# Kernel tuning notes

Hardware: AMD Instinct MI355X
Metric: run time of the kernel (lower is better)

Reference implementation:

```python
import jax, jax.numpy as jnp
import numpy as np

GRID_SIZE = 5
SPLINE_ORDER = 3
ALPHA = 0.2


def _make_grid(in_features, dtype=jnp.float32):
    # uniform grid on [-1, 1] extended by spline_order on each side
    h = 2.0 / GRID_SIZE
    pts = jnp.arange(-SPLINE_ORDER, GRID_SIZE + SPLINE_ORDER + 1, dtype=dtype) * h - 1.0
    return jnp.broadcast_to(pts, (in_features, pts.shape[0]))  # [in, G+2k+1]


def _b_splines(x, grid):
    # x: [N, in] -> bases: [N, in, GRID_SIZE + SPLINE_ORDER]
    x = x[..., None]  # [N, in, 1]
    bases = ((x >= grid[:, :-1]) & (x < grid[:, 1:])).astype(x.dtype)
    for k in range(1, SPLINE_ORDER + 1):
        left = (x - grid[:, : -(k + 1)]) / (grid[:, k:-1] - grid[:, : -(k + 1)])
        right = (grid[:, k + 1 :] - x) / (grid[:, k + 1 :] - grid[:, 1:-k])
        bases = left * bases[..., :-1] + right * bases[..., 1:]
    return bases


def _kan(x, base_weight, spline_weight):
    # efficient-KAN layer: silu base linear + B-spline linear
    N, Fin = x.shape
    Fout = base_weight.shape[0]
    grid = _make_grid(Fin, x.dtype)
    bases = _b_splines(x, grid)  # [N, in, C]
    base_out = jax.nn.silu(x) @ base_weight.T
    spline_out = bases.reshape(N, -1) @ spline_weight.reshape(Fout, -1).T
    return base_out + spline_out


def setup_inputs() -> dict:
    key = jax.random.key(0)
    k1, k2, k3, k4, k5, k6 = jax.random.split(key, 6)
    N, E, Fin, Fout = 50000, 800000, 128, 128
    C = GRID_SIZE + SPLINE_ORDER
    h = jax.random.normal(k1, (N, Fin), dtype=jnp.float32)
    edge_index = jax.random.randint(k2, (2, E), 0, N, dtype=jnp.int64)
    W = jax.random.normal(k3, (Fin, Fout), dtype=jnp.float32) * (1.414 / np.sqrt(Fin))
    a = jax.random.normal(k4, (2 * Fout, 1), dtype=jnp.float32) * 0.1
    base_weight = jax.random.normal(k5, (Fout, Fin), dtype=jnp.float32) / np.sqrt(Fin)
    spline_weight = jax.random.normal(k6, (Fout, Fin, C), dtype=jnp.float32) * 0.1
    return {"h": h, "edge_index": edge_index, "W": W, "a": a,
            "base_weight": base_weight, "spline_weight": spline_weight}


def reference(h, edge_index, W, a, base_weight, spline_weight):
    N = h.shape[0]
    Fout = W.shape[1]
    HW = h @ W                                # [N, Fout]
    HW_KAN = _kan(h, base_weight, spline_weight)  # [N, Fout]
    row, col = edge_index[0], edge_index[1]
    # cat([HW_i, HW_j]) @ a == HW_i @ a[:Fout] + HW_j @ a[Fout:]; precompute per node
    s_src = HW @ a[:Fout, 0]                  # [N]
    s_dst = HW @ a[Fout:, 0]                  # [N]
    e = jax.nn.leaky_relu(s_src[row] + s_dst[col], ALPHA)  # [E]
    # segment softmax grouped by row
    m = jax.ops.segment_max(e, row, num_segments=N)
    e_exp = jnp.exp(e - m[row])
    denom = jax.ops.segment_sum(e_exp, row, num_segments=N)
    att = e_exp / denom[row]                  # [E] (dropout inactive in eval)
    out = jax.ops.segment_sum(att[:, None] * HW_KAN[col], row, num_segments=N)
    return out
```

## Files before the change

### kernel.cpp

```cpp
#include <hip/hip_runtime.h>
#include <hip/hip_bf16.h>
#include <math.h>

#define NCHUNK 9
#define BM 128
#define NTHR 512
#define PREPB ((NCHUNK * 128 * 128) / 256)

typedef __attribute__((ext_vector_type(4))) float f32x4;
typedef __attribute__((ext_vector_type(8))) short bf16x8;
typedef unsigned int u32;
typedef unsigned long long u64;

__device__ __forceinline__ unsigned short f2bf(float f) {
    u32 u = __builtin_bit_cast(u32, f);
    u32 r = (u + 0x7FFFu + ((u >> 16) & 1u)) >> 16;
    return (unsigned short)r;
}

__device__ __forceinline__ float siluf(float x) {
    return x / (1.0f + __expf(-x));
}

__global__ void k_prep(const float* __restrict__ bw, const float* __restrict__ sw,
                       const float* __restrict__ W, const float* __restrict__ a,
                       unsigned short* __restrict__ Bsw, float* __restrict__ wa,
                       const int* __restrict__ erow, int* __restrict__ counts, int E) {
    int bid = blockIdx.x;
    if (bid < PREPB) {
        int i = bid * 256 + threadIdx.x;
        int j = i & 7;
        int s = (i >> 3) & 15;
        int o = (i >> 7) & 127;
        int c = i >> 14;
        int k = c * 128 + (((s ^ (o & 7)) << 3) | j);
        float v = (k < 128) ? bw[o * 128 + k] : sw[o * 1024 + (k - 128)];
        Bsw[i] = f2bf(v);
        return;
    }
    if (bid == PREPB) {
        int fi = threadIdx.x;
        if (fi < 128) {
            float s1 = 0.f, s2 = 0.f;
            for (int o = 0; o < 128; ++o) {
                float w = W[fi * 128 + o];
                s1 = fmaf(w, a[o], s1);
                s2 = fmaf(w, a[128 + o], s2);
            }
            wa[fi] = s1;
            wa[128 + fi] = s2;
        }
        return;
    }
    int e = (bid - PREPB - 1) * 256 + threadIdx.x;
    if (e < E) atomicAdd(&counts[erow[e]], 1);
}

__global__ __launch_bounds__(NTHR) void k_nodes(const float* __restrict__ h,
                                                const unsigned short* __restrict__ Bsw,
                                                const float* __restrict__ wa,
                                                unsigned short* __restrict__ kanb,
                                                float* __restrict__ s_src,
                                                float* __restrict__ s_dst, int N, int nbn,
                                                const int* __restrict__ erow,
                                                const int* __restrict__ ecol,
                                                const int* __restrict__ offsets,
                                                int* __restrict__ cursor,
                                                int* __restrict__ colss, int E) {
    __shared__ unsigned short A_lds[BM * 128];
    __shared__ unsigned short B_lds[128 * 128];
    const int tid = threadIdx.x;

    if (blockIdx.x >= nbn) {
        int e = (blockIdx.x - nbn) * NTHR + tid;
        if (e < E) {
            int r = erow[e];
            int pos = offsets[r] + atomicAdd(&cursor[r], 1);
            colss[pos] = ecol[e];
        }
        return;
    }

    const int wid = tid >> 6, lane = tid & 63;
    const int gm0 = blockIdx.x * BM;

    const int gm = tid >> 2, gq = tid & 3;
    const float* ghr = h + (size_t)min(gm0 + gm, N - 1) * 128;

    const int wm0 = (wid >> 1) * 32;
    const int wn0 = (wid & 1) * 64;
    f32x4 acc[2][4];
#pragma unroll
    for (int im = 0; im < 2; ++im)
#pragma unroll
        for (int in = 0; in < 4; ++in) acc[im][in] = {0.f, 0.f, 0.f, 0.f};

    f32x4 pf = {0.f, 0.f, 0.f, 0.f};
    for (int chunk = 0; chunk < NCHUNK; ++chunk) {
        {
            const char* gsrc = (const char*)Bsw + (size_t)chunk * 32768 + wid * 4096 + lane * 16;
            char* ldst = (char*)B_lds + wid * 4096;
#pragma unroll
            for (int i = 0; i < 4; ++i) {
                __builtin_amdgcn_global_load_lds(
                    (const __attribute__((address_space(1))) u32*)(gsrc + i * 1024),
                    (__attribute__((address_space(3))) u32*)(ldst + i * 1024), 16, 0, 0);
            }
        }
        f32x4 pfn = pf;
        if (chunk <= 7) pfn = *(const f32x4*)(ghr + chunk * 16 + gq * 4);

        if (chunk == 0) {
            f32x4 xv[8];
#pragma unroll
            for (int v = 0; v < 8; ++v) xv[v] = *(const f32x4*)(ghr + gq * 32 + v * 4);
#pragma unroll
            for (int sl = 0; sl < 4; ++sl) {
                int s = gq * 4 + sl;
                unsigned short pk[8];
#pragma unroll
                for (int j = 0; j < 4; ++j) {
                    pk[j] = f2bf(siluf(xv[2 * sl][j]));
                    pk[4 + j] = f2bf(siluf(xv[2 * sl + 1][j]));
                }
                *(bf16x8*)((char*)A_lds + gm * 256 + (((s ^ (gm & 7)) & 15) << 4)) =
                    *(bf16x8*)pk;
            }
        } else {
#pragma unroll
            for (int j = 0; j < 4; ++j) {
                float x = pf[j];
                float t = (x + 2.2f) * 2.5f;
                float fl = floorf(t);
                int i0 = (int)fl;
                float u = t - fl;
                float um = 1.0f - u;
                float u2 = u * u, u3 = u2 * u;
                const float c6 = 1.0f / 6.0f;
                float w0 = um * um * um * c6;
                float w1 = (3.f * u3 - 6.f * u2 + 4.f) * c6;
                float w2 = (-3.f * u3 + 3.f * u2 + 3.f * u + 1.f) * c6;
                float w3 = u3 * c6;
                u64 Wp = (u64)f2bf(w0) | ((u64)f2bf(w1) << 16) |
                         ((u64)f2bf(w2) << 32) | ((u64)f2bf(w3) << 48);
                int sh = (i0 - 3) * 16;
                u64 lo = 0, hi = 0;
                if (sh >= 0) {
                    if (sh < 64) {
                        lo = Wp << sh;
                        hi = sh ? (Wp >> (64 - sh)) : 0;
                    } else if (sh < 128) {
                        hi = Wp << (sh - 64);
                    }
                } else {
                    int r = -sh;
                    if (r < 64) lo = Wp >> r;
                }
                int s = gq * 4 + j;
                ulonglong2 pv; pv.x = lo; pv.y = hi;
                *(ulonglong2*)((char*)A_lds + gm * 256 + (((s ^ (gm & 7)) & 15) << 4)) = pv;
            }
        }
        __syncthreads();

#pragma unroll
        for (int kk = 0; kk < 4; ++kk) {
            bf16x8 af[2], bfr[4];
#pragma unroll
            for (int im = 0; im < 2; ++im) {
                int mrow = wm0 + im * 16 + (lane & 15);
                int slot = (kk * 4 + (lane >> 4)) ^ (mrow & 7);
                af[im] = *(const bf16x8*)((const char*)A_lds + mrow * 256 + slot * 16);
            }
#pragma unroll
            for (int in = 0; in < 4; ++in) {
                int orow = wn0 + in * 16 + (lane & 15);
                int slot = (kk * 4 + (lane >> 4)) ^ (orow & 7);
                bfr[in] = *(const bf16x8*)((const char*)B_lds + orow * 256 + slot * 16);
            }
#pragma unroll
            for (int im = 0; im < 2; ++im)
#pragma unroll
                for (int in = 0; in < 4; ++in)
                    acc[im][in] = __builtin_amdgcn_mfma_f32_16x16x32_bf16(
                        af[im], bfr[in], acc[im][in], 0, 0, 0);
        }
        __syncthreads();
        pf = pfn;
    }

    float wa0 = wa[lane], wa1 = wa[64 + lane];
    float wa2 = wa[128 + lane], wa3 = wa[192 + lane];
    float sx0[16], sx1[16];
    const int r0 = gm0 + wid * 16;
#pragma unroll
    for (int rr = 0; rr < 16; ++rr) {
        const float* hr = h + (size_t)min(r0 + rr, N - 1) * 128;
        sx0[rr] = hr[lane];
        sx1[rr] = hr[64 + lane];
    }

#pragma unroll
    for (int im = 0; im < 2; ++im) {
        int rbase = wm0 + im * 16 + ((lane >> 4) << 2);
#pragma unroll
        for (int in = 0; in < 4; ++in) {
            int col = wn0 + in * 16 + (lane & 15);
#pragma unroll
            for (int r = 0; r < 4; ++r) {
                int row = rbase + r;
                int byte = row * 256 + ((col * 2) ^ ((row & 7) << 4));
                *(unsigned short*)((char*)A_lds + byte) = f2bf(acc[im][in][r]);
            }
        }
    }
    __syncthreads();
    for (int i = tid; i < BM * 16; i += NTHR) {
        int row = i >> 4, s = i & 15;
        int byte = row * 256 + ((s << 4) ^ ((row & 7) << 4));
        bf16x8 v = *(bf16x8*)((char*)A_lds + byte);
        int grow = gm0 + row;
        if (grow < N) *(bf16x8*)((char*)kanb + (size_t)grow * 256 + s * 16) = v;
    }

#pragma unroll
    for (int rr = 0; rr < 16; ++rr) {
        float s1 = fmaf(sx0[rr], wa0, sx1[rr] * wa1);
        float s2 = fmaf(sx0[rr], wa2, sx1[rr] * wa3);
#pragma unroll
        for (int off = 32; off; off >>= 1) {
            s1 += __shfl_xor(s1, off, 64);
            s2 += __shfl_xor(s2, off, 64);
        }
        int grow = r0 + rr;
        if (lane == 0 && grow < N) {
            s_src[grow] = s1;
            s_dst[grow] = s2;
        }
    }
}

__global__ void k_scan1(const int* __restrict__ counts, int* __restrict__ bsum, int N) {
    int tid = threadIdx.x;
    int idx = blockIdx.x * 256 + tid;
    int v = (idx < N) ? counts[idx] : 0;
#pragma unroll
    for (int off = 32; off; off >>= 1) v += __shfl_xor(v, off, 64);
    __shared__ int ws[4];
    if ((tid & 63) == 0) ws[tid >> 6] = v;
    __syncthreads();
    if (tid == 0) bsum[blockIdx.x] = ws[0] + ws[1] + ws[2] + ws[3];
}

__global__ __launch_bounds__(1024) void k_scan2(const int* __restrict__ bsum,
                                                int* __restrict__ ebase,
                                                int* __restrict__ offsN, int nb) {
    __shared__ int ws[16];
    __shared__ int tot;
    int tid = threadIdx.x;
    int lane = tid & 63, w = tid >> 6;
    int v = (tid < nb) ? bsum[tid] : 0;
    int inc = v;
#pragma unroll
    for (int off = 1; off < 64; off <<= 1) {
        int t = __shfl_up(inc, off, 64);
        if (lane >= off) inc += t;
    }
    if (lane == 63) ws[w] = inc;
    __syncthreads();
    if (w == 0 && lane < 16) {
        int x = ws[lane];
#pragma unroll
        for (int off = 1; off < 16; off <<= 1) {
            int t = __shfl_up(x, off, 64);
            if (lane >= off) x += t;
        }
        ws[lane] = x;
        if (lane == 15) tot = x;
    }
    __syncthreads();
    int wb = w ? ws[w - 1] : 0;
    if (tid < nb) ebase[tid] = wb + inc - v;
    if (tid == 0) offsN[0] = tot;
}

__global__ void k_scan3(const int* __restrict__ counts, const int* __restrict__ ebase,
                        int* __restrict__ offsets, int N) {
    int tid = threadIdx.x;
    int idx = blockIdx.x * 256 + tid;
    int v = (idx < N) ? counts[idx] : 0;
    int lane = tid & 63, w = tid >> 6;
    int inc = v;
#pragma unroll
    for (int off = 1; off < 64; off <<= 1) {
        int t = __shfl_up(inc, off, 64);
        if (lane >= off) inc += t;
    }
    __shared__ int ws[4];
    if (lane == 63) ws[w] = inc;
    __syncthreads();
    int wb = 0;
    for (int i = 0; i < w; ++i) wb += ws[i];
    if (idx < N) offsets[idx] = ebase[blockIdx.x] + wb + inc - v;
}

__global__ __launch_bounds__(256) void k_aggr(const int* __restrict__ offsets,
                                              int* __restrict__ cols,
                                              const float* __restrict__ s_src,
                                              const float* __restrict__ s_dst,
                                              const unsigned short* __restrict__ kanb,
                                              float* __restrict__ out, int N) {
    int wid = (blockIdx.x * 256 + threadIdx.x) >> 6;
    int lane = threadIdx.x & 63;
    if (wid >= N) return;
    int start = offsets[wid], end = offsets[wid + 1];
    int deg = end - start;
    float acc0 = 0.f, acc1 = 0.f;
    if (deg > 0) {
        float ssrc = s_src[wid];
        if (deg <= 64) {
            int key = 0x7fffffff;
            if (lane < deg) key = cols[start + lane];
#pragma unroll
            for (int k = 2; k <= 64; k <<= 1) {
#pragma unroll
                for (int j = k >> 1; j > 0; j >>= 1) {
                    int other = __shfl_xor(key, j, 64);
                    bool asc = ((lane & k) == 0);
                    bool lowr = ((lane & j) == 0);
                    int mn = min(key, other), mx = max(key, other);
                    key = (asc == lowr) ? mn : mx;
                }
            }
            float e = -3.402823466e38f;
            if (lane < deg) {
                e = ssrc + s_dst[key];
                e = (e >= 0.f) ? e : 0.2f * e;
            }
            float m = e;
#pragma unroll
            for (int off = 32; off; off >>= 1) m = fmaxf(m, __shfl_xor(m, off, 64));
            float ex = (lane < deg) ? __expf(e - m) : 0.f;
            float s = ex;
#pragma unroll
            for (int off = 32; off; off >>= 1) s += __shfl_xor(s, off, 64);
            float att = ex / s;
            for (int q0 = 0; q0 < deg; q0 += 4) {
                float w[4];
                u32 p[4];
#pragma unroll
                for (int t = 0; t < 4; ++t) {
                    int q = q0 + t;
                    int c = __shfl(key, q < deg ? q : 0, 64);
                    float wt = __shfl(att, q < 64 ? q : 0, 64);
                    w[t] = (q < deg) ? wt : 0.f;
                    p[t] = ((const u32*)(kanb + (size_t)c * 128))[lane];
                }
#pragma unroll
                for (int t = 0; t < 4; ++t) {
                    float lo = __builtin_bit_cast(float, p[t] << 16);
                    float hi = __builtin_bit_cast(float, p[t] & 0xffff0000u);
                    acc0 = fmaf(w[t], lo, acc0);
                    acc1 = fmaf(w[t], hi, acc1);
                }
            }
        } else {
            if (lane == 0) {
                for (int i = start + 1; i < end; ++i) {
                    int v = cols[i];
                    int j = i - 1;
                    while (j >= start && cols[j] > v) { cols[j + 1] = cols[j]; --j; }
                    cols[j + 1] = v;
                }
            }
            __threadfence();
            float m = -3.402823466e38f;
            for (int j = start + lane; j < end; j += 64) {
                float e = ssrc + s_dst[cols[j]];
                e = (e >= 0.f) ? e : 0.2f * e;
                m = fmaxf(m, e);
            }
#pragma unroll
            for (int off = 32; off; off >>= 1) m = fmaxf(m, __shfl_xor(m, off, 64));
            float s = 0.f;
            for (int j = start + lane; j < end; j += 64) {
                float e = ssrc + s_dst[cols[j]];
                e = (e >= 0.f) ? e : 0.2f * e;
                s += __expf(e - m);
            }
#pragma unroll
            for (int off = 32; off; off >>= 1) s += __shfl_xor(s, off, 64);
            float inv = 1.0f / s;
            for (int t = start; t < end; t += 64) {
                int j = t + lane;
                float att = 0.f;
                int myc = 0;
                if (j < end) {
                    myc = cols[j];
                    float e = ssrc + s_dst[myc];
                    e = (e >= 0.f) ? e : 0.2f * e;
                    att = __expf(e - m) * inv;
                }
                int cnt = min(64, end - t);
                for (int q = 0; q < cnt; ++q) {
                    float w = __shfl(att, q, 64);
                    int c = __shfl(myc, q, 64);
                    u32 p = ((const u32*)(kanb + (size_t)c * 128))[lane];
                    float lo = __builtin_bit_cast(float, p << 16);
                    float hi = __builtin_bit_cast(float, p & 0xffff0000u);
                    acc0 = fmaf(w, lo, acc0);
                    acc1 = fmaf(w, hi, acc1);
                }
            }
        }
    }
    float2 o2 = make_float2(acc0, acc1);
    *(float2*)(out + (size_t)wid * 128 + lane * 2) = o2;
}

extern "C" void kernel_launch(void* const* d_in, const int* in_sizes, int n_in,
                              void* d_out, int out_size, void* d_ws, size_t ws_size,
                              hipStream_t stream) {
    const float* h  = (const float*)d_in[0];
    const int*   ei = (const int*)d_in[1];
    const float* W  = (const float*)d_in[2];
    const float* a  = (const float*)d_in[3];
    const float* bw = (const float*)d_in[4];
    const float* sw = (const float*)d_in[5];
    float* out = (float*)d_out;
    const int N = in_sizes[0] / 128;
    const int E = in_sizes[1] / 2;
    const int nb = (N + 255) / 256;
    const int nbn = (N + BM - 1) / BM;
    const int nbs = (E + NTHR - 1) / NTHR;
    const int nbh = (E + 255) / 256;

    char* ws = (char*)d_ws;
    auto alloc = [&](size_t bytes) {
        char* p = ws;
        ws += (bytes + 255) & ~(size_t)255;
        return p;
    };
    unsigned short* Bsw = (unsigned short*)alloc((size_t)NCHUNK * 128 * 128 * 2);
    float* wa    = (float*)alloc(256 * 4);
    float* ssrc  = (float*)alloc((size_t)N * 4);
    float* sdst  = (float*)alloc((size_t)N * 4);
    unsigned short* kanb = (unsigned short*)alloc((size_t)N * 128 * 2);
    int* counts  = (int*)alloc((size_t)N * 4);
    int* cursor  = (int*)alloc((size_t)N * 4);
    int* offsets = (int*)alloc(((size_t)N + 1) * 4);
    int* colss   = (int*)alloc((size_t)E * 4);
    int* bsum    = (int*)alloc((size_t)nb * 4);
    int* ebase   = (int*)alloc((size_t)nb * 4);

    hipMemsetAsync(counts, 0, (size_t)N * 4, stream);
    hipMemsetAsync(cursor, 0, (size_t)N * 4, stream);

    k_prep<<<PREPB + 1 + nbh, 256, 0, stream>>>(bw, sw, W, a, Bsw, wa, ei, counts, E);
    k_scan1<<<nb, 256, 0, stream>>>(counts, bsum, N);
    k_scan2<<<1, 1024, 0, stream>>>(bsum, ebase, offsets + N, nb);
    k_scan3<<<nb, 256, 0, stream>>>(counts, ebase, offsets, N);
    k_nodes<<<nbn + nbs, NTHR, 0, stream>>>(h, Bsw, wa, kanb, ssrc, sdst, N, nbn,
                                            ei, ei + E, offsets, cursor, colss, E);
    k_aggr<<<(N + 3) / 4, 256, 0, stream>>>(offsets, colss, ssrc, sdst, kanb, out, N);
}
```

Measured before the change: 148.3 us.

## Software-pipeline neighbor gathers, change LDS swizzle, merge memsets

The aggregation loop now gathers neighbor features in batches of 8 and prefetches the next batch while the current one is accumulated, so more global loads are in flight to hide gather latency. The LDS XOR swizzle used when staging the KAN output tile is changed to a pattern keyed on row groups, aimed at fewer bank conflicts on the bf16 stores and reads. The two memsets of counts and cursor are merged into one call, relying on the two buffers being contiguous in the workspace. The prefetch raises register pressure and issues extra padded loads when degree is below 8.

```diff
diff --git a/kernel.cpp b/kernel.cpp
--- a/kernel.cpp
+++ b/kernel.cpp
@@ -209,7 +209,7 @@
 #pragma unroll
             for (int r = 0; r < 4; ++r) {
                 int row = rbase + r;
-                int byte = row * 256 + ((col * 2) ^ ((row & 7) << 4));
+                int byte = row * 256 + ((col * 2) ^ (((row >> 2) & 3) << 5));
                 *(unsigned short*)((char*)A_lds + byte) = f2bf(acc[im][in][r]);
             }
         }
@@ -217,7 +217,7 @@
     __syncthreads();
     for (int i = tid; i < BM * 16; i += NTHR) {
         int row = i >> 4, s = i & 15;
-        int byte = row * 256 + ((s << 4) ^ ((row & 7) << 4));
+        int byte = row * 256 + ((s << 4) ^ (((row >> 2) & 3) << 5));
         bf16x8 v = *(bf16x8*)((char*)A_lds + byte);
         int grow = gm0 + row;
         if (grow < N) *(bf16x8*)((char*)kanb + (size_t)grow * 256 + s * 16) = v;
@@ -345,23 +345,36 @@
 #pragma unroll
             for (int off = 32; off; off >>= 1) s += __shfl_xor(s, off, 64);
             float att = ex / s;
-            for (int q0 = 0; q0 < deg; q0 += 4) {
-                float w[4];
-                u32 p[4];
-#pragma unroll
-                for (int t = 0; t < 4; ++t) {
-                    int q = q0 + t;
-                    int c = __shfl(key, q < deg ? q : 0, 64);
-                    float wt = __shfl(att, q < 64 ? q : 0, 64);
-                    w[t] = (q < deg) ? wt : 0.f;
-                    p[t] = ((const u32*)(kanb + (size_t)c * 128))[lane];
-                }
-#pragma unroll
-                for (int t = 0; t < 4; ++t) {
-                    float lo = __builtin_bit_cast(float, p[t] << 16);
-                    float hi = __builtin_bit_cast(float, p[t] & 0xffff0000u);
-                    acc0 = fmaf(w[t], lo, acc0);
-                    acc1 = fmaf(w[t], hi, acc1);
+            u32 pbuf[8];
+            float wbuf[8];
+#pragma unroll
+            for (int t = 0; t < 8; ++t) {
+                int qc = (t < deg) ? t : 0;
+                int c = __shfl(key, qc, 64);
+                wbuf[t] = (t < deg) ? __shfl(att, qc, 64) : 0.f;
+                pbuf[t] = ((const u32*)(kanb + (size_t)c * 128))[lane];
+            }
+            for (int q0 = 0; q0 < deg; q0 += 8) {
+                u32 pc[8];
+                float wc[8];
+#pragma unroll
+                for (int t = 0; t < 8; ++t) { pc[t] = pbuf[t]; wc[t] = wbuf[t]; }
+                if (q0 + 8 < deg) {
+#pragma unroll
+                    for (int t = 0; t < 8; ++t) {
+                        int q = q0 + 8 + t;
+                        int qc = (q < deg) ? q : 0;
+                        int c = __shfl(key, qc, 64);
+                        wbuf[t] = (q < deg) ? __shfl(att, qc, 64) : 0.f;
+                        pbuf[t] = ((const u32*)(kanb + (size_t)c * 128))[lane];
+                    }
+                }
+#pragma unroll
+                for (int t = 0; t < 8; ++t) {
+                    float lo = __builtin_bit_cast(float, pc[t] << 16);
+                    float hi = __builtin_bit_cast(float, pc[t] & 0xffff0000u);
+                    acc0 = fmaf(wc[t], lo, acc0);
+                    acc1 = fmaf(wc[t], hi, acc1);
                 }
             }
         } else {
@@ -453,8 +466,8 @@
     int* bsum    = (int*)alloc((size_t)nb * 4);
     int* ebase   = (int*)alloc((size_t)nb * 4);
 
-    hipMemsetAsync(counts, 0, (size_t)N * 4, stream);
-    hipMemsetAsync(cursor, 0, (size_t)N * 4, stream);
+    size_t npad = ((size_t)N * 4 + 255) & ~(size_t)255;
+    hipMemsetAsync(counts, 0, npad + (size_t)N * 4, stream);
 
     k_prep<<<PREPB + 1 + nbh, 256, 0, stream>>>(bw, sw, W, a, Bsw, wa, ei, counts, E);
     k_scan1<<<nb, 256, 0, stream>>>(counts, bsum, N);
```

Measured after the change: 147.9 us. Within noise of the previous version (-0.3%).
